# Optimization experiments

Hardware: AMD Instinct MI355X
Metric: run time of the kernel (lower is better)

## Reference

```python
import jax, jax.numpy as jnp
import numpy as np

N = 4194304  # number of points (== number of edges)
M = 16384    # number of clusters


def setup_inputs() -> dict:
    key = jax.random.key(0)
    k1, k2, k3, k4, k5, k6 = jax.random.split(key, 6)
    x = jax.random.normal(k1, (N, 3), dtype=jnp.float32)
    pos = jax.random.normal(k2, (N, 3), dtype=jnp.float32)
    batch = jnp.zeros((N,), dtype=jnp.int64)
    cluster_weights = jax.random.uniform(k3, (M, 1), dtype=jnp.float32)
    R = jax.random.normal(k4, (M, 3, 3), dtype=jnp.float32)
    t = jax.random.normal(k5, (M, 3), dtype=jnp.float32)
    point_idx = jnp.arange(N, dtype=jnp.int64)
    cluster_idx = jax.random.randint(k6, (N,), 0, M, dtype=jnp.int64)
    edge_index = jnp.stack([point_idx, cluster_idx], axis=0)
    return {"x": x, "pos": pos, "batch": batch,
            "cluster_weights": cluster_weights, "R": R, "t": t,
            "edge_index": edge_index}


def reference(x, pos, batch, cluster_weights, R, t, edge_index):
    cluster_idx = edge_index[1]
    # gather per-edge rotation / translation / weight
    R_point = R[cluster_idx]            # [N, 3, 3]
    t_point = t[cluster_idx]            # [N, 3]
    # tiny batched 3x3 matmul + add
    x_pred = jnp.einsum('eij,ej->ei', R_point, pos) + t_point  # [N, 3]
    point_weights = cluster_weights[cluster_idx]               # [N, 1]
    x_out = x * point_weights + x_pred * (1.0 - point_weights)
    return (R_point, t_point, x_out)
```

## Files before the change

kernel.cpp:

```cpp
#include <hip/hip_runtime.h>


typedef float f4 __attribute__((ext_vector_type(4)));

__global__ void __launch_bounds__(256)
prepack_kernel(const float* __restrict__ cw,
               const float* __restrict__ Rm,
               const float* __restrict__ tm,
               float* __restrict__ packed,
               int M)
{
    int i = blockIdx.x * 256 + threadIdx.x;
    if (i >= M * 16) return;
    int r = i >> 4, j = i & 15;
    float v = 0.0f;
    if (j < 9)       v = Rm[r * 9 + j];
    else if (j < 12) v = tm[r * 3 + (j - 9)];
    else if (j == 12) v = cw[r];
    packed[i] = v;
}

__global__ void __launch_bounds__(256)
transf_prop_kernel(const float* __restrict__ x,
                   const float* __restrict__ pos,
                   const float* __restrict__ packed,
                   const int*   __restrict__ cidx,
                   float* __restrict__ Rp,
                   float* __restrict__ tp,
                   float* __restrict__ xo,
                   int n)
{
    __shared__ __align__(16) float s_pos[768];
    __shared__ __align__(16) float s_x[768];
    __shared__ __align__(16) float s_R[2304];
    __shared__ __align__(16) float s_t[768];
    __shared__ __align__(16) float s_o[768];

    const int t    = threadIdx.x;
    const int base = blockIdx.x * 256;

    if (base + 256 <= n) {
        const int c = cidx[base + t];
        const f4* row = (const f4*)(packed + (size_t)c * 16);
        const f4 q0 = row[0];
        const f4 q1 = row[1];
        const f4 q2 = row[2];
        const f4 q3 = row[3];

        const f4* pos4 = (const f4*)(pos + (size_t)base * 3);
        const f4* x4   = (const f4*)(x   + (size_t)base * 3);
        if (t < 192) {
            ((f4*)s_pos)[t] = pos4[t];
            ((f4*)s_x)[t]   = x4[t];
        }
        __syncthreads();

        const float p0 = s_pos[t * 3 + 0];
        const float p1 = s_pos[t * 3 + 1];
        const float p2 = s_pos[t * 3 + 2];
        const float x0 = s_x[t * 3 + 0];
        const float x1 = s_x[t * 3 + 1];
        const float x2 = s_x[t * 3 + 2];

        const float pr0 = fmaf(q0.x, p0, fmaf(q0.y, p1, fmaf(q0.z, p2, q2.y)));
        const float pr1 = fmaf(q0.w, p0, fmaf(q1.x, p1, fmaf(q1.y, p2, q2.z)));
        const float pr2 = fmaf(q1.z, p0, fmaf(q1.w, p1, fmaf(q2.x, p2, q2.w)));
        const float w   = q3.x;
        const float omw = 1.0f - w;

        s_R[t * 9 + 0] = q0.x; s_R[t * 9 + 1] = q0.y; s_R[t * 9 + 2] = q0.z;
        s_R[t * 9 + 3] = q0.w; s_R[t * 9 + 4] = q1.x; s_R[t * 9 + 5] = q1.y;
        s_R[t * 9 + 6] = q1.z; s_R[t * 9 + 7] = q1.w; s_R[t * 9 + 8] = q2.x;
        s_t[t * 3 + 0] = q2.y;
        s_t[t * 3 + 1] = q2.z;
        s_t[t * 3 + 2] = q2.w;
        s_o[t * 3 + 0] = fmaf(x0, w, pr0 * omw);
        s_o[t * 3 + 1] = fmaf(x1, w, pr1 * omw);
        s_o[t * 3 + 2] = fmaf(x2, w, pr2 * omw);
        __syncthreads();

        f4* Rb4 = (f4*)(Rp + (size_t)base * 9);
        const f4* sR4 = (const f4*)s_R;
        __builtin_nontemporal_store(sR4[t],       &Rb4[t]);
        __builtin_nontemporal_store(sR4[t + 256], &Rb4[t + 256]);
        if (t < 64)
            __builtin_nontemporal_store(sR4[t + 512], &Rb4[t + 512]);

        f4* tb4 = (f4*)(tp + (size_t)base * 3);
        f4* ob4 = (f4*)(xo + (size_t)base * 3);
        if (t < 192) {
            __builtin_nontemporal_store(((const f4*)s_t)[t], &tb4[t]);
            __builtin_nontemporal_store(((const f4*)s_o)[t], &ob4[t]);
        }
    } else {
        const int m  = n - base;
        const int m3 = m * 3, m9 = m * 9;
        const float* posb = pos + (size_t)base * 3;
        const float* xb   = x   + (size_t)base * 3;
        for (int k = 0; k < 3; ++k) {
            int i = t + 256 * k;
            if (i < m3) { s_pos[i] = posb[i]; s_x[i] = xb[i]; }
        }
        __syncthreads();
        if (t < m) {
            const int c = cidx[base + t];
            const float* row = packed + (size_t)c * 16;
            float r[9];
            for (int j = 0; j < 9; ++j) r[j] = row[j];
            const float t0 = row[9], t1 = row[10], t2 = row[11];
            const float w  = row[12];
            const float p0 = s_pos[t*3], p1 = s_pos[t*3+1], p2 = s_pos[t*3+2];
            const float x0 = s_x[t*3],   x1 = s_x[t*3+1],   x2 = s_x[t*3+2];
            const float pr0 = fmaf(r[0], p0, fmaf(r[1], p1, fmaf(r[2], p2, t0)));
            const float pr1 = fmaf(r[3], p0, fmaf(r[4], p1, fmaf(r[5], p2, t1)));
            const float pr2 = fmaf(r[6], p0, fmaf(r[7], p1, fmaf(r[8], p2, t2)));
            const float omw = 1.0f - w;
            for (int j = 0; j < 9; ++j) s_R[t * 9 + j] = r[j];
            s_t[t*3] = t0; s_t[t*3+1] = t1; s_t[t*3+2] = t2;
            s_o[t*3]   = fmaf(x0, w, pr0 * omw);
            s_o[t*3+1] = fmaf(x1, w, pr1 * omw);
            s_o[t*3+2] = fmaf(x2, w, pr2 * omw);
        }
        __syncthreads();
        float* Rb = Rp + (size_t)base * 9;
        for (int k = 0; k < 9; ++k) {
            int i = t + 256 * k;
            if (i < m9) __builtin_nontemporal_store(s_R[i], &Rb[i]);
        }
        float* tb = tp + (size_t)base * 3;
        float* ob = xo + (size_t)base * 3;
        for (int k = 0; k < 3; ++k) {
            int i = t + 256 * k;
            if (i < m3) {
                __builtin_nontemporal_store(s_t[i], &tb[i]);
                __builtin_nontemporal_store(s_o[i], &ob[i]);
            }
        }
    }
}

extern "C" void kernel_launch(void* const* d_in, const int* in_sizes, int n_in,
                              void* d_out, int out_size, void* d_ws, size_t ws_size,
                              hipStream_t stream) {
    const float* x   = (const float*)d_in[0];
    const float* pos = (const float*)d_in[1];
    const float* cw  = (const float*)d_in[3];
    const float* Rm  = (const float*)d_in[4];
    const float* tm  = (const float*)d_in[5];
    const int*  edge = (const int*)d_in[6];

    const int n = in_sizes[0] / 3;
    const int M = in_sizes[3];
    const int* cidx = edge + n;

    float* out = (float*)d_out;
    float* Rp = out;
    float* tp = out + (size_t)n * 9;
    float* xo = out + (size_t)n * 12;

    float* packed = (float*)d_ws;

    const int block = 256;
    const int pgrid = (M * 16 + block - 1) / block;
    prepack_kernel<<<pgrid, block, 0, stream>>>(cw, Rm, tm, packed, M);

    const int grid = (n + block - 1) / block;
    transf_prop_kernel<<<grid, block, 0, stream>>>(x, pos, packed, cidx,
                                                   Rp, tp, xo, n);
}
```

Baseline: 63.25 us.

## Cooperatively gather packed cluster rows with four threads per point

Each group of four lanes now loads the four 16-byte chunks of one cluster's packed row, instead of one thread loading all 64 bytes. This makes the random gathers touch contiguous 64-byte segments per lane group, for better memory coalescing. The 3x3 matvec is split across lanes and combined with xor shuffles, and the weight is broadcast with a shuffle. The cost is extra shuffle and divergent-branch work, plus shared-memory stores done in four passes.

```diff
diff --git a/kernel.cpp b/kernel.cpp
--- a/kernel.cpp
+++ b/kernel.cpp
@@ -40,12 +40,18 @@
     const int base = blockIdx.x * 256;
 
     if (base + 256 <= n) {
-        const int c = cidx[base + t];
-        const f4* row = (const f4*)(packed + (size_t)c * 16);
-        const f4 q0 = row[0];
-        const f4 q1 = row[1];
-        const f4 q2 = row[2];
-        const f4 q3 = row[3];
+        const int sub = t >> 2;
+        const int q   = t & 3;
+
+        const int c0 = cidx[base +       sub];
+        const int c1 = cidx[base +  64 + sub];
+        const int c2 = cidx[base + 128 + sub];
+        const int c3 = cidx[base + 192 + sub];
+        const f4* pk4 = (const f4*)packed;
+        const f4 row0 = pk4[(size_t)c0 * 4 + q];
+        const f4 row1 = pk4[(size_t)c1 * 4 + q];
+        const f4 row2 = pk4[(size_t)c2 * 4 + q];
+        const f4 row3 = pk4[(size_t)c3 * 4 + q];
 
         const f4* pos4 = (const f4*)(pos + (size_t)base * 3);
         const f4* x4   = (const f4*)(x   + (size_t)base * 3);
@@ -55,28 +61,46 @@
         }
         __syncthreads();
 
-        const float p0 = s_pos[t * 3 + 0];
-        const float p1 = s_pos[t * 3 + 1];
-        const float p2 = s_pos[t * 3 + 2];
-        const float x0 = s_x[t * 3 + 0];
-        const float x1 = s_x[t * 3 + 1];
-        const float x2 = s_x[t * 3 + 2];
+        #pragma unroll
+        for (int g = 0; g < 4; ++g) {
+            const int pt = g * 64 + sub;
+            const f4 v = (g == 0) ? row0 : (g == 1) ? row1 : (g == 2) ? row2 : row3;
 
-        const float pr0 = fmaf(q0.x, p0, fmaf(q0.y, p1, fmaf(q0.z, p2, q2.y)));
-        const float pr1 = fmaf(q0.w, p0, fmaf(q1.x, p1, fmaf(q1.y, p2, q2.z)));
-        const float pr2 = fmaf(q1.z, p0, fmaf(q1.w, p1, fmaf(q2.x, p2, q2.w)));
-        const float w   = q3.x;
-        const float omw = 1.0f - w;
+            if (q == 0) {
+                s_R[9*pt+0] = v.x; s_R[9*pt+1] = v.y;
+                s_R[9*pt+2] = v.z; s_R[9*pt+3] = v.w;
+            } else if (q == 1) {
+                s_R[9*pt+4] = v.x; s_R[9*pt+5] = v.y;
+                s_R[9*pt+6] = v.z; s_R[9*pt+7] = v.w;
+            } else if (q == 2) {
+                s_R[9*pt+8] = v.x;
+                s_t[3*pt+0] = v.y; s_t[3*pt+1] = v.z; s_t[3*pt+2] = v.w;
+            }
 
-        s_R[t * 9 + 0] = q0.x; s_R[t * 9 + 1] = q0.y; s_R[t * 9 + 2] = q0.z;
-        s_R[t * 9 + 3] = q0.w; s_R[t * 9 + 4] = q1.x; s_R[t * 9 + 5] = q1.y;
-        s_R[t * 9 + 6] = q1.z; s_R[t * 9 + 7] = q1.w; s_R[t * 9 + 8] = q2.x;
-        s_t[t * 3 + 0] = q2.y;
-        s_t[t * 3 + 1] = q2.z;
-        s_t[t * 3 + 2] = q2.w;
-        s_o[t * 3 + 0] = fmaf(x0, w, pr0 * omw);
-        s_o[t * 3 + 1] = fmaf(x1, w, pr1 * omw);
-        s_o[t * 3 + 2] = fmaf(x2, w, pr2 * omw);
+            const float p0 = s_pos[3*pt+0], p1 = s_pos[3*pt+1], p2 = s_pos[3*pt+2];
+            float a0 = 0.f, a1 = 0.f, a2 = 0.f;
+            if (q == 0) {
+                a0 = fmaf(v.x, p0, fmaf(v.y, p1, v.z * p2));
+                a1 = v.w * p0;
+            } else if (q == 1) {
+                a1 = fmaf(v.x, p1, v.y * p2);
+                a2 = fmaf(v.z, p0, v.w * p1);
+            } else if (q == 2) {
+                a0 = v.y;
+                a1 = v.z;
+                a2 = fmaf(v.x, p2, v.w);
+            }
+            a0 += __shfl_xor(a0, 1); a1 += __shfl_xor(a1, 1); a2 += __shfl_xor(a2, 1);
+            a0 += __shfl_xor(a0, 2); a1 += __shfl_xor(a1, 2); a2 += __shfl_xor(a2, 2);
+            const float w   = __shfl(v.x, t | 3);
+            const float omw = 1.0f - w;
+
+            if (q < 3) {
+                const float pr = (q == 0) ? a0 : (q == 1) ? a1 : a2;
+                const float xv = s_x[3*pt+q];
+                s_o[3*pt+q] = fmaf(xv, w, pr * omw);
+            }
+        }
         __syncthreads();
 
         f4* Rb4 = (f4*)(Rp + (size_t)base * 9);
```

Measured after the change: 65.30 us. 3.2% more time.
